# Performance work log

Hardware: AMD Instinct MI355X
Metric: run time of the kernel (lower is better)

The kernel has to match this reference:

```python
import jax, jax.numpy as jnp
import numpy as np

EPS = 1e-6

def _cos_sim_matrix(a, b, eps=EPS):
    # a: (N, D), b: (M, D) -> (N, M), matches torch CosineSimilarity semantics:
    # dot / max(||a||*||b||, eps)
    dots = a @ b.T
    na = jnp.sqrt(jnp.sum(a * a, axis=1))
    nb = jnp.sqrt(jnp.sum(b * b, axis=1))
    return dots / jnp.maximum(na[:, None] * nb[None, :], eps)

def setup_inputs() -> dict:
    key = jax.random.key(0)
    k1, k2, k3 = jax.random.split(key, 3)
    B, L, D = 4096, 1024, 256
    f = jax.random.normal(k1, (B, L), dtype=jnp.float32)
    noise = jax.random.normal(k2, (B, L), dtype=jnp.float32)
    ref = jax.random.normal(k3, (B, D), dtype=jnp.float32)
    return {"f": f, "noise": noise, "ref": ref}

def reference(f, noise, ref):
    B = f.shape[0]
    cat_f_agent = jnp.concatenate([noise, f], axis=0)              # (2B, L)
    matrix = jnp.exp(_cos_sim_matrix(f, cat_f_agent))              # (B, 2B)

    ref2 = jnp.concatenate([ref, ref], axis=0)                     # (2B, D)
    # weight for negative pair (i, j): (1 - cos_sim(ref_i, ref_j)) / 2
    weight = (1.0 - _cos_sim_matrix(ref, ref2)) * 0.5              # (B, 2B)

    idx = jnp.arange(B)
    # exclude j == i (positive pair) and j == i + B (self pair)
    mask = jnp.ones((B, 2 * B), dtype=matrix.dtype)
    mask = mask.at[idx, idx].set(0.0)
    mask = mask.at[idx, idx + B].set(0.0)

    positive_pairs = matrix[idx, idx]                              # (B,)
    negative_sum = jnp.sum(matrix * weight * mask, axis=-1)        # (B,)

    loss = -jnp.log(positive_pairs / (negative_sum + EPS))
    return loss.mean()
```

## Files before the change

### kernel.cpp

```cpp
#include <hip/hip_runtime.h>
#include <hip/hip_bf16.h>
#include <math.h>

#define BDIM 4096
#define LDIM 1024
#define DDIM 256
#define EPSF 1e-6f

typedef unsigned short ushort_t;
typedef __attribute__((ext_vector_type(8))) short short8;
typedef __attribute__((ext_vector_type(4))) float floatx4;
typedef __attribute__((ext_vector_type(2))) _Float16 half2v;

__device__ inline ushort_t f2bf(float x) {
    union { __hip_bfloat16 h; ushort_t u; } v;
    v.h = __float2bfloat16(x);
    return v.u;
}

__device__ inline void gl2lds16(const ushort_t* g, ushort_t* l) {
    __builtin_amdgcn_global_load_lds(
        (const __attribute__((address_space(1))) void*)g,
        (__attribute__((address_space(3))) void*)l,
        16, 0, 0);
}

__device__ inline void reduce_atomic(float (&rowsum)[4][4], float* __restrict__ neg,
                                     int base_i, int quad, int l16)
{
    #pragma unroll
    for (int off = 1; off < 16; off <<= 1)
        #pragma unroll
        for (int mi = 0; mi < 4; ++mi)
            #pragma unroll
            for (int r = 0; r < 4; ++r)
                rowsum[mi][r] += __shfl_xor(rowsum[mi][r], off, 64);
    if (l16 == 0) {
        #pragma unroll
        for (int mi = 0; mi < 4; ++mi)
            #pragma unroll
            for (int r = 0; r < 4; ++r)
                atomicAdd(&neg[base_i + mi * 16 + quad * 4 + r], rowsum[mi][r]);
    }
}

__global__ __launch_bounds__(256) void prep_kernel(
    const float* __restrict__ f, const float* __restrict__ noise,
    const float* __restrict__ ref,
    ushort_t* __restrict__ catb, ushort_t* __restrict__ refb,
    float* __restrict__ incat, float* __restrict__ inr,
    float* __restrict__ neg)
{
    const int b = blockIdx.x;
    const int wv = threadIdx.x >> 6, lane = threadIdx.x & 63;
    if (b < 2048) {
        const int row = b * 4 + wv;
        const float* src = (row < BDIM) ? noise + (size_t)row * LDIM
                                        : f + (size_t)(row - BDIM) * LDIM;
        ushort_t* dst = catb + (size_t)row * LDIM;
        float s = 0.f;
        #pragma unroll
        for (int t = 0; t < 4; ++t) {
            float4 v = *(const float4*)(src + t * 256 + lane * 4);
            s += v.x * v.x + v.y * v.y + v.z * v.z + v.w * v.w;
            ushort4 o = { f2bf(v.x), f2bf(v.y), f2bf(v.z), f2bf(v.w) };
            *(ushort4*)(dst + t * 256 + lane * 4) = o;
        }
        #pragma unroll
        for (int off = 32; off > 0; off >>= 1) s += __shfl_down(s, off, 64);
        if (lane == 0) incat[row] = 1.0f / sqrtf(s);
    } else {
        const int row = (b - 2048) * 4 + wv;
        float4 v = *(const float4*)(ref + (size_t)row * DDIM + lane * 4);
        float s = v.x * v.x + v.y * v.y + v.z * v.z + v.w * v.w;
        ushort4 o = { f2bf(v.x), f2bf(v.y), f2bf(v.z), f2bf(v.w) };
        *(ushort4*)(refb + (size_t)row * DDIM + lane * 4) = o;
        #pragma unroll
        for (int off = 32; off > 0; off >>= 1) s += __shfl_down(s, off, 64);
        if (lane == 0) inr[row] = 1.0f / sqrtf(s);
        if (threadIdx.x == 0)
            *(float4*)(neg + (size_t)(b - 2048) * 4) = (float4){0.f, 0.f, 0.f, 0.f};
    }
}

__global__ __launch_bounds__(256, 2) void pair_mfma(
    const ushort_t* __restrict__ catb,
    const ushort_t* __restrict__ refb,
    const float* __restrict__ incat,
    const float* __restrict__ inr,
    float* __restrict__ neg, float* __restrict__ pos)
{
    __shared__ __align__(16) ushort_t As [128 * 64];
    __shared__ __align__(16) ushort_t Bs1[128 * 64];
    __shared__ __align__(16) ushort_t Bs2[128 * 64];

    const int tid = threadIdx.x;
    const int wid = tid >> 6, ln = tid & 63;
    const int i0 = blockIdx.y * 128;
    const int jm0 = blockIdx.x * 128;
    const int wm = (wid >> 1) * 64, wn = (wid & 1) * 64;
    const int quad = ln >> 4, l16 = ln & 15;

    const int lrow = ln >> 3;
    const int scol = ((ln & 7) ^ lrow) * 8;

    half2v wpack[4][4][2];
    {
        floatx4 accw[4][4];
        #pragma unroll
        for (int a = 0; a < 4; ++a)
            #pragma unroll
            for (int c = 0; c < 4; ++c) accw[a][c] = (floatx4){0.f, 0.f, 0.f, 0.f};
        const ushort_t* A2 = refb + (size_t)i0 * DDIM;
        const ushort_t* B2 = refb + (size_t)jm0 * DDIM;
        for (int k0 = 0; k0 < DDIM; k0 += 64) {
            __syncthreads();
            #pragma unroll
            for (int t = 0; t < 4; ++t) {
                const int row0 = wid * 32 + t * 8;
                gl2lds16(A2 + (size_t)(row0 + lrow) * DDIM + k0 + scol, As  + row0 * 64);
                gl2lds16(B2 + (size_t)(row0 + lrow) * DDIM + k0 + scol, Bs1 + row0 * 64);
            }
            __syncthreads();
            #pragma unroll
            for (int kk = 0; kk < 2; ++kk) {
                const int sw = ((kk * 4 + quad) ^ (l16 & 7)) * 8;
                short8 af[4], bf[4];
                #pragma unroll
                for (int mi = 0; mi < 4; ++mi)
                    af[mi] = *(const short8*)(As + (wm + mi * 16 + l16) * 64 + sw);
                #pragma unroll
                for (int ni = 0; ni < 4; ++ni)
                    bf[ni] = *(const short8*)(Bs1 + (wn + ni * 16 + l16) * 64 + sw);
                #pragma unroll
                for (int mi = 0; mi < 4; ++mi)
                    #pragma unroll
                    for (int ni = 0; ni < 4; ++ni)
                        accw[mi][ni] = __builtin_amdgcn_mfma_f32_16x16x32_bf16(
                            af[mi], bf[ni], accw[mi][ni], 0, 0, 0);
            }
        }
        float irow[4], icol[4];
        #pragma unroll
        for (int ni = 0; ni < 4; ++ni)
            icol[ni] = inr[jm0 + wn + ni * 16 + l16];
        #pragma unroll
        for (int mi = 0; mi < 4; ++mi) {
            #pragma unroll
            for (int r = 0; r < 4; ++r)
                irow[r] = inr[i0 + wm + mi * 16 + quad * 4 + r];
            #pragma unroll
            for (int ni = 0; ni < 4; ++ni) {
                float w0 = (1.0f - accw[mi][ni][0] * irow[0] * icol[ni]) * 0.5f;
                float w1 = (1.0f - accw[mi][ni][1] * irow[1] * icol[ni]) * 0.5f;
                float w2 = (1.0f - accw[mi][ni][2] * irow[2] * icol[ni]) * 0.5f;
                float w3 = (1.0f - accw[mi][ni][3] * irow[3] * icol[ni]) * 0.5f;
                wpack[mi][ni][0] = (half2v){ (_Float16)w0, (_Float16)w1 };
                wpack[mi][ni][1] = (half2v){ (_Float16)w2, (_Float16)w3 };
            }
        }
    }

    floatx4 acc1[4][4], acc2[4][4];
    #pragma unroll
    for (int a = 0; a < 4; ++a)
        #pragma unroll
        for (int c = 0; c < 4; ++c) {
            acc1[a][c] = (floatx4){0.f, 0.f, 0.f, 0.f};
            acc2[a][c] = (floatx4){0.f, 0.f, 0.f, 0.f};
        }
    {
        const ushort_t* Ag  = catb + (size_t)(BDIM + i0) * LDIM;
        const ushort_t* B1g = catb + (size_t)jm0 * LDIM;
        const ushort_t* B2g = catb + (size_t)(BDIM + jm0) * LDIM;
        for (int k0 = 0; k0 < LDIM; k0 += 64) {
            __syncthreads();
            #pragma unroll
            for (int t = 0; t < 4; ++t) {
                const int row0 = wid * 32 + t * 8;
                const size_t go = (size_t)(row0 + lrow) * LDIM + k0 + scol;
                gl2lds16(Ag  + go, As  + row0 * 64);
                gl2lds16(B1g + go, Bs1 + row0 * 64);
                gl2lds16(B2g + go, Bs2 + row0 * 64);
            }
            __syncthreads();
            #pragma unroll
            for (int kk = 0; kk < 2; ++kk) {
                const int sw = ((kk * 4 + quad) ^ (l16 & 7)) * 8;
                short8 af[4], bf1[4], bf2[4];
                #pragma unroll
                for (int mi = 0; mi < 4; ++mi)
                    af[mi] = *(const short8*)(As + (wm + mi * 16 + l16) * 64 + sw);
                #pragma unroll
                for (int ni = 0; ni < 4; ++ni) {
                    bf1[ni] = *(const short8*)(Bs1 + (wn + ni * 16 + l16) * 64 + sw);
                    bf2[ni] = *(const short8*)(Bs2 + (wn + ni * 16 + l16) * 64 + sw);
                }
                #pragma unroll
                for (int mi = 0; mi < 4; ++mi)
                    #pragma unroll
                    for (int ni = 0; ni < 4; ++ni) {
                        acc1[mi][ni] = __builtin_amdgcn_mfma_f32_16x16x32_bf16(
                            af[mi], bf1[ni], acc1[mi][ni], 0, 0, 0);
                        acc2[mi][ni] = __builtin_amdgcn_mfma_f32_16x16x32_bf16(
                            af[mi], bf2[ni], acc2[mi][ni], 0, 0, 0);
                    }
            }
        }
    }

    {
        float ifi[4][4], injn[4], injf[4];
        #pragma unroll
        for (int mi = 0; mi < 4; ++mi)
            #pragma unroll
            for (int r = 0; r < 4; ++r)
                ifi[mi][r] = incat[BDIM + i0 + wm + mi * 16 + quad * 4 + r];
        #pragma unroll
        for (int ni = 0; ni < 4; ++ni) {
            injn[ni] = incat[jm0 + wn + ni * 16 + l16];
            injf[ni] = incat[BDIM + jm0 + wn + ni * 16 + l16];
        }
        float rowsum[4][4];
        #pragma unroll
        for (int mi = 0; mi < 4; ++mi)
            #pragma unroll
            for (int r = 0; r < 4; ++r) rowsum[mi][r] = 0.f;
        #pragma unroll
        for (int mi = 0; mi < 4; ++mi)
            #pragma unroll
            for (int ni = 0; ni < 4; ++ni)
                #pragma unroll
                for (int r = 0; r < 4; ++r) {
                    int gi = i0 + wm + mi * 16 + quad * 4 + r;
                    int gc = jm0 + wn + ni * 16 + l16;
                    float e1 = __expf(acc1[mi][ni][r] * ifi[mi][r] * injn[ni]);
                    float e2 = __expf(acc2[mi][ni][r] * ifi[mi][r] * injf[ni]);
                    float w = (float)wpack[mi][ni][r >> 1][r & 1];
                    if (gc == gi) pos[gi] = e1;
                    else rowsum[mi][r] += w * (e1 + e2);
                }
        reduce_atomic(rowsum, neg, i0 + wm, quad, l16);
    }
}

__global__ __launch_bounds__(256) void finalize_kernel(const float* __restrict__ neg,
                                                       const float* __restrict__ pos,
                                                       float* __restrict__ out) {
    float s = 0.f;
    for (int i = threadIdx.x; i < BDIM; i += 256)
        s += logf(neg[i] + EPSF) - logf(pos[i]);
    #pragma unroll
    for (int off = 32; off > 0; off >>= 1) s += __shfl_down(s, off, 64);
    __shared__ float ws[4];
    int lane = threadIdx.x & 63, wid = threadIdx.x >> 6;
    if (lane == 0) ws[wid] = s;
    __syncthreads();
    if (threadIdx.x == 0) out[0] = (ws[0] + ws[1] + ws[2] + ws[3]) / (float)BDIM;
}

extern "C" void kernel_launch(void* const* d_in, const int* in_sizes, int n_in,
                              void* d_out, int out_size, void* d_ws, size_t ws_size,
                              hipStream_t stream) {
    const float* f     = (const float*)d_in[0];
    const float* noise = (const float*)d_in[1];
    const float* ref   = (const float*)d_in[2];
    float* out = (float*)d_out;

    char* w = (char*)d_ws;
    ushort_t* catb = (ushort_t*)w;
    ushort_t* refb = (ushort_t*)(w + (size_t)16777216);
    float* incat   = (float*)(w + (size_t)18874368);
    float* inr     = (float*)(w + (size_t)18907136);
    float* neg     = (float*)(w + (size_t)18923520);
    float* pos     = (float*)(w + (size_t)18939904);

    prep_kernel<<<3072, 256, 0, stream>>>(f, noise, ref, catb, refb, incat, inr, neg);

    dim3 grid(BDIM / 128, BDIM / 128);
    pair_mfma<<<grid, 256, 0, stream>>>(catb, refb, incat, inr, neg, pos);

    finalize_kernel<<<1, 256, 0, stream>>>(neg, pos, out);
}
```

Measured before the change: 178.2 us.

## Switch GEMM operands from bf16 to fp8 with fp8 MFMA

Quantizes the concatenated feature rows and the ref rows to fp8 (e4m3 via cvt_pk_fp8) in the prep kernel instead of bf16. The pair kernel then uses 16x16x32 fp8 MFMA with 128-byte K tiles and a reworked swizzled LDS addressing scheme. This halves global and LDS traffic and the number of K iterations, and aims for higher MFMA throughput. The cost is much lower precision in the cosine dot products, which are then exponentiated, so accuracy against the reference may suffer.

After: 166.0 us. -6.8%, faster.

```diff
diff --git a/kernel.cpp b/kernel.cpp
--- a/kernel.cpp
+++ b/kernel.cpp
@@ -7,24 +7,23 @@
 #define DDIM 256
 #define EPSF 1e-6f
 
-typedef unsigned short ushort_t;
-typedef __attribute__((ext_vector_type(8))) short short8;
+typedef unsigned char uchar_t;
 typedef __attribute__((ext_vector_type(4))) float floatx4;
 typedef __attribute__((ext_vector_type(2))) _Float16 half2v;
 
-__device__ inline ushort_t f2bf(float x) {
-    union { __hip_bfloat16 h; ushort_t u; } v;
-    v.h = __float2bfloat16(x);
-    return v.u;
-}
-
-__device__ inline void gl2lds16(const ushort_t* g, ushort_t* l) {
+__device__ inline void gl2lds16(const uchar_t* g, uchar_t* l) {
     __builtin_amdgcn_global_load_lds(
         (const __attribute__((address_space(1))) void*)g,
         (__attribute__((address_space(3))) void*)l,
         16, 0, 0);
 }
 
+__device__ inline unsigned int pk4_fp8(float4 v) {
+    unsigned int p = __builtin_amdgcn_cvt_pk_fp8_f32(v.x, v.y, 0u, false);
+    p = __builtin_amdgcn_cvt_pk_fp8_f32(v.z, v.w, p, true);
+    return p;
+}
+
 __device__ inline void reduce_atomic(float (&rowsum)[4][4], float* __restrict__ neg,
                                      int base_i, int quad, int l16)
 {
@@ -47,7 +46,7 @@
 __global__ __launch_bounds__(256) void prep_kernel(
     const float* __restrict__ f, const float* __restrict__ noise,
     const float* __restrict__ ref,
-    ushort_t* __restrict__ catb, ushort_t* __restrict__ refb,
+    uchar_t* __restrict__ catb, uchar_t* __restrict__ refb,
     float* __restrict__ incat, float* __restrict__ inr,
     float* __restrict__ neg)
 {
@@ -57,14 +56,13 @@
         const int row = b * 4 + wv;
         const float* src = (row < BDIM) ? noise + (size_t)row * LDIM
                                         : f + (size_t)(row - BDIM) * LDIM;
-        ushort_t* dst = catb + (size_t)row * LDIM;
+        uchar_t* dst = catb + (size_t)row * LDIM;
         float s = 0.f;
         #pragma unroll
         for (int t = 0; t < 4; ++t) {
             float4 v = *(const float4*)(src + t * 256 + lane * 4);
             s += v.x * v.x + v.y * v.y + v.z * v.z + v.w * v.w;
-            ushort4 o = { f2bf(v.x), f2bf(v.y), f2bf(v.z), f2bf(v.w) };
-            *(ushort4*)(dst + t * 256 + lane * 4) = o;
+            *(unsigned int*)(dst + t * 256 + lane * 4) = pk4_fp8(v);
         }
         #pragma unroll
         for (int off = 32; off > 0; off >>= 1) s += __shfl_down(s, off, 64);
@@ -73,8 +71,7 @@
         const int row = (b - 2048) * 4 + wv;
         float4 v = *(const float4*)(ref + (size_t)row * DDIM + lane * 4);
         float s = v.x * v.x + v.y * v.y + v.z * v.z + v.w * v.w;
-        ushort4 o = { f2bf(v.x), f2bf(v.y), f2bf(v.z), f2bf(v.w) };
-        *(ushort4*)(refb + (size_t)row * DDIM + lane * 4) = o;
+        *(unsigned int*)(refb + (size_t)row * DDIM + lane * 4) = pk4_fp8(v);
         #pragma unroll
         for (int off = 32; off > 0; off >>= 1) s += __shfl_down(s, off, 64);
         if (lane == 0) inr[row] = 1.0f / sqrtf(s);
@@ -84,15 +81,15 @@
 }
 
 __global__ __launch_bounds__(256, 2) void pair_mfma(
-    const ushort_t* __restrict__ catb,
-    const ushort_t* __restrict__ refb,
+    const uchar_t* __restrict__ catb,
+    const uchar_t* __restrict__ refb,
     const float* __restrict__ incat,
     const float* __restrict__ inr,
     float* __restrict__ neg, float* __restrict__ pos)
 {
-    __shared__ __align__(16) ushort_t As [128 * 64];
-    __shared__ __align__(16) ushort_t Bs1[128 * 64];
-    __shared__ __align__(16) ushort_t Bs2[128 * 64];
+    __shared__ __align__(16) uchar_t As [128 * 128];
+    __shared__ __align__(16) uchar_t Bs1[128 * 128];
+    __shared__ __align__(16) uchar_t Bs2[128 * 128];
 
     const int tid = threadIdx.x;
     const int wid = tid >> 6, ln = tid & 63;
@@ -102,7 +99,12 @@
     const int quad = ln >> 4, l16 = ln & 15;
 
     const int lrow = ln >> 3;
-    const int scol = ((ln & 7) ^ lrow) * 8;
+    const int scol = ((ln & 7) ^ lrow) * 16;
+
+    int co[4];
+    #pragma unroll
+    for (int kk = 0; kk < 4; ++kk)
+        co[kk] = (((2 * kk + (quad >> 1)) ^ (l16 & 7)) * 16) + (quad & 1) * 8;
 
     half2v wpack[4][4][2];
     {
@@ -111,32 +113,31 @@
         for (int a = 0; a < 4; ++a)
             #pragma unroll
             for (int c = 0; c < 4; ++c) accw[a][c] = (floatx4){0.f, 0.f, 0.f, 0.f};
-        const ushort_t* A2 = refb + (size_t)i0 * DDIM;
-        const ushort_t* B2 = refb + (size_t)jm0 * DDIM;
-        for (int k0 = 0; k0 < DDIM; k0 += 64) {
+        const uchar_t* A2 = refb + (size_t)i0 * DDIM;
+        const uchar_t* B2 = refb + (size_t)jm0 * DDIM;
+        for (int k0 = 0; k0 < DDIM; k0 += 128) {
             __syncthreads();
             #pragma unroll
             for (int t = 0; t < 4; ++t) {
                 const int row0 = wid * 32 + t * 8;
-                gl2lds16(A2 + (size_t)(row0 + lrow) * DDIM + k0 + scol, As  + row0 * 64);
-                gl2lds16(B2 + (size_t)(row0 + lrow) * DDIM + k0 + scol, Bs1 + row0 * 64);
-            }
-            __syncthreads();
-            #pragma unroll
-            for (int kk = 0; kk < 2; ++kk) {
-                const int sw = ((kk * 4 + quad) ^ (l16 & 7)) * 8;
-                short8 af[4], bf[4];
-                #pragma unroll
-                for (int mi = 0; mi < 4; ++mi)
-                    af[mi] = *(const short8*)(As + (wm + mi * 16 + l16) * 64 + sw);
+                gl2lds16(A2 + (size_t)(row0 + lrow) * DDIM + k0 + scol, As  + row0 * 128);
+                gl2lds16(B2 + (size_t)(row0 + lrow) * DDIM + k0 + scol, Bs1 + row0 * 128);
+            }
+            __syncthreads();
+            #pragma unroll
+            for (int kk = 0; kk < 4; ++kk) {
+                long af[4], bf[4];
+                #pragma unroll
+                for (int mi = 0; mi < 4; ++mi)
+                    af[mi] = *(const long*)(As + (wm + mi * 16 + l16) * 128 + co[kk]);
                 #pragma unroll
                 for (int ni = 0; ni < 4; ++ni)
-                    bf[ni] = *(const short8*)(Bs1 + (wn + ni * 16 + l16) * 64 + sw);
+                    bf[ni] = *(const long*)(Bs1 + (wn + ni * 16 + l16) * 128 + co[kk]);
                 #pragma unroll
                 for (int mi = 0; mi < 4; ++mi)
                     #pragma unroll
                     for (int ni = 0; ni < 4; ++ni)
-                        accw[mi][ni] = __builtin_amdgcn_mfma_f32_16x16x32_bf16(
+                        accw[mi][ni] = __builtin_amdgcn_mfma_f32_16x16x32_fp8_fp8(
                             af[mi], bf[ni], accw[mi][ni], 0, 0, 0);
             }
         }
@@ -170,39 +171,38 @@
             acc2[a][c] = (floatx4){0.f, 0.f, 0.f, 0.f};
         }
     {
-        const ushort_t* Ag  = catb + (size_t)(BDIM + i0) * LDIM;
-        const ushort_t* B1g = catb + (size_t)jm0 * LDIM;
-        const ushort_t* B2g = catb + (size_t)(BDIM + jm0) * LDIM;
-        for (int k0 = 0; k0 < LDIM; k0 += 64) {
+        const uchar_t* Ag  = catb + (size_t)(BDIM + i0) * LDIM;
+        const uchar_t* B1g = catb + (size_t)jm0 * LDIM;
+        const uchar_t* B2g = catb + (size_t)(BDIM + jm0) * LDIM;
+        for (int k0 = 0; k0 < LDIM; k0 += 128) {
             __syncthreads();
             #pragma unroll
             for (int t = 0; t < 4; ++t) {
                 const int row0 = wid * 32 + t * 8;
                 const size_t go = (size_t)(row0 + lrow) * LDIM + k0 + scol;
-                gl2lds16(Ag  + go, As  + row0 * 64);
-                gl2lds16(B1g + go, Bs1 + row0 * 64);
-                gl2lds16(B2g + go, Bs2 + row0 * 64);
-            }
-            __syncthreads();
-            #pragma unroll
-            for (int kk = 0; kk < 2; ++kk) {
-                const int sw = ((kk * 4 + quad) ^ (l16 & 7)) * 8;
-                short8 af[4], bf1[4], bf2[4];
-                #pragma unroll
-                for (int mi = 0; mi < 4; ++mi)
-                    af[mi] = *(const short8*)(As + (wm + mi * 16 + l16) * 64 + sw);
+                gl2lds16(Ag  + go, As  + row0 * 128);
+                gl2lds16(B1g + go, Bs1 + row0 * 128);
+                gl2lds16(B2g + go, Bs2 + row0 * 128);
+            }
+            __syncthreads();
+            #pragma unroll
+            for (int kk = 0; kk < 4; ++kk) {
+                long af[4], bf1[4], bf2[4];
+                #pragma unroll
+                for (int mi = 0; mi < 4; ++mi)
+                    af[mi] = *(const long*)(As + (wm + mi * 16 + l16) * 128 + co[kk]);
                 #pragma unroll
                 for (int ni = 0; ni < 4; ++ni) {
-                    bf1[ni] = *(const short8*)(Bs1 + (wn + ni * 16 + l16) * 64 + sw);
-                    bf2[ni] = *(const short8*)(Bs2 + (wn + ni * 16 + l16) * 64 + sw);
+                    bf1[ni] = *(const long*)(Bs1 + (wn + ni * 16 + l16) * 128 + co[kk]);
+                    bf2[ni] = *(const long*)(Bs2 + (wn + ni * 16 + l16) * 128 + co[kk]);
                 }
                 #pragma unroll
                 for (int mi = 0; mi < 4; ++mi)
                     #pragma unroll
                     for (int ni = 0; ni < 4; ++ni) {
-                        acc1[mi][ni] = __builtin_amdgcn_mfma_f32_16x16x32_bf16(
+                        acc1[mi][ni] = __builtin_amdgcn_mfma_f32_16x16x32_fp8_fp8(
                             af[mi], bf1[ni], acc1[mi][ni], 0, 0, 0);
-                        acc2[mi][ni] = __builtin_amdgcn_mfma_f32_16x16x32_bf16(
+                        acc2[mi][ni] = __builtin_amdgcn_mfma_f32_16x16x32_fp8_fp8(
                             af[mi], bf2[ni], acc2[mi][ni], 0, 0, 0);
                     }
             }
@@ -268,12 +268,12 @@
     float* out = (float*)d_out;
 
     char* w = (char*)d_ws;
-    ushort_t* catb = (ushort_t*)w;
-    ushort_t* refb = (ushort_t*)(w + (size_t)16777216);
-    float* incat   = (float*)(w + (size_t)18874368);
-    float* inr     = (float*)(w + (size_t)18907136);
-    float* neg     = (float*)(w + (size_t)18923520);
-    float* pos     = (float*)(w + (size_t)18939904);
+    uchar_t* catb = (uchar_t*)w;
+    uchar_t* refb = (uchar_t*)(w + (size_t)8388608);
+    float* incat  = (float*)(w + (size_t)9437184);
+    float* inr    = (float*)(w + (size_t)9469952);
+    float* neg    = (float*)(w + (size_t)9486336);
+    float* pos    = (float*)(w + (size_t)9502720);
 
     prep_kernel<<<3072, 256, 0, stream>>>(f, noise, ref, catb, refb, incat, inr, neg);
 
```
